# Kernel tuning notes

Hardware: AMD Instinct MI355X
Metric: run time of the kernel (lower is better)

Reference implementation:

```python
import jax, jax.numpy as jnp
import numpy as np

DIM = 1024
EXPANSION = 4
NUM_EXPERTS = 8
N_TOKENS = 4096
CAPACITY_FACTOR = 1.0  # also becomes the gate's k -> top-1 (bug-faithful)
EPS = 1e-6


def setup_inputs() -> dict:
    key = jax.random.key(0)
    ks = jax.random.split(key, 7)
    h = DIM * EXPANSION
    s = 0.02
    return {
        "x": jax.random.normal(ks[0], (N_TOKENS, DIM), dtype=jnp.float32),
        "w_gate": jax.random.normal(ks[1], (DIM, NUM_EXPERTS), dtype=jnp.float32) * s,
        "b_gate": jnp.zeros((NUM_EXPERTS,), dtype=jnp.float32),
        "w1": jax.random.normal(ks[2], (NUM_EXPERTS, DIM, h), dtype=jnp.float32) * s,
        "b1": jnp.zeros((NUM_EXPERTS, h), dtype=jnp.float32),
        "w2": jax.random.normal(ks[3], (NUM_EXPERTS, h, DIM), dtype=jnp.float32) * s,
        "b2": jnp.zeros((NUM_EXPERTS, DIM), dtype=jnp.float32),
    }


def fast_gelu(x):
    return x * jax.nn.sigmoid(1.702 * x)


def switch_gate(x, w_gate, b_gate):
    # x: [n, d] -> gate_scores: [n, e]
    gate_scores = jax.nn.softmax(x @ w_gate + b_gate, axis=-1)
    capacity = int(CAPACITY_FACTOR * x.shape[0])
    k = int(CAPACITY_FACTOR)  # SwitchMoE passes capacity_factor as k -> top-1
    _, top_k_idx = jax.lax.top_k(gate_scores, k)  # [n, k]
    mask = jnp.zeros_like(gate_scores).at[
        jnp.arange(x.shape[0])[:, None], top_k_idx
    ].set(1.0)
    masked = gate_scores * mask
    denom = masked.sum(axis=0, keepdims=True) + EPS  # [1, e]
    gate_scores = masked / denom * capacity
    # aux loss (use_aux_loss=True in SwitchMoE)
    load = gate_scores.sum(axis=0)               # [e]
    importance = gate_scores.sum(axis=1).mean()  # scalar
    loss = jnp.mean((load - importance) ** 2)
    return gate_scores, loss


def reference(x, w_gate, b_gate, w1, b1, w2, b2):
    gate_scores, loss = switch_gate(x, w_gate, b_gate)  # [n, e], scalar
    # dense compute-all-experts (faithful to the naive module)
    h = fast_gelu(jnp.einsum("nd,edh->enh", x, w1) + b1[:, None, :])  # [e, n, h]
    expert_out = jnp.einsum("enh,ehd->end", h, w2) + b2[:, None, :]   # [e, n, d]
    # weighted combine: sum_e gate[n,e] * expert_out[e,n,d]
    moe_output = jnp.einsum("ne,end->nd", gate_scores, expert_out)
    return moe_output, loss
```

## Files before the change

### kernel.cpp

```cpp
#include <hip/hip_runtime.h>
#include <hip/hip_bf16.h>
#include <math.h>

#define DIMK   1024
#define HDIM   4096
#define NEXP   8
#define NTOK   4096
#define EPSV   1e-6f

typedef __attribute__((ext_vector_type(4))) float  f32x4;
typedef __attribute__((ext_vector_type(8))) __bf16 bf16x8;
typedef __attribute__((ext_vector_type(4))) __bf16 bf16x4;

__device__ __forceinline__ __bf16 f2bf(float f) { return (__bf16)f; }

__device__ __forceinline__ void gload_lds16(const void* g, void* l) {
    __builtin_amdgcn_global_load_lds(
        (const __attribute__((address_space(1))) void*)g,
        (__attribute__((address_space(3))) void*)l, 16, 0, 0);
}

__global__ void init_kernel(int* counts, int* cursors, float* S) {
    int t = threadIdx.x;
    if (t < NEXP) { counts[t] = 0; cursors[t] = 0; S[t] = 0.0f; }
}

__global__ __launch_bounds__(256) void gate_kernel(
    const float* __restrict__ x, const float* __restrict__ wg,
    const float* __restrict__ bg,
    float* S, int* counts, float* score_top, int* texp)
{
    int n = blockIdx.x;
    int t = threadIdx.x;
    f32x4 xv = *(const f32x4*)(x + (size_t)n * DIMK + t * 4);

    float p[NEXP];
#pragma unroll
    for (int e = 0; e < NEXP; e++) p[e] = 0.0f;
#pragma unroll
    for (int j = 0; j < 4; j++) {
        int d = t * 4 + j;
        f32x4 wa = *(const f32x4*)(wg + (size_t)d * NEXP);
        f32x4 wb = *(const f32x4*)(wg + (size_t)d * NEXP + 4);
#pragma unroll
        for (int e = 0; e < 4; e++) { p[e] += xv[j] * wa[e]; p[e + 4] += xv[j] * wb[e]; }
    }
#pragma unroll
    for (int e = 0; e < NEXP; e++) {
#pragma unroll
        for (int off = 32; off > 0; off >>= 1)
            p[e] += __shfl_down(p[e], off, 64);
    }
    __shared__ float red[4][NEXP];
    int lane = t & 63, wv = t >> 6;
    if (lane == 0) {
#pragma unroll
        for (int e = 0; e < NEXP; e++) red[wv][e] = p[e];
    }
    __syncthreads();
    if (t == 0) {
        float l[NEXP]; float m = -1e30f;
#pragma unroll
        for (int e = 0; e < NEXP; e++) {
            l[e] = red[0][e] + red[1][e] + red[2][e] + red[3][e] + bg[e];
            m = fmaxf(m, l[e]);
        }
        float pe[NEXP]; float s = 0.0f;
#pragma unroll
        for (int e = 0; e < NEXP; e++) { pe[e] = __expf(l[e] - m); s += pe[e]; }
        int best = 0; float bv = pe[0];
#pragma unroll
        for (int e = 1; e < NEXP; e++) if (pe[e] > bv) { bv = pe[e]; best = e; }
        float sc = bv / s;
        score_top[n] = sc;
        texp[n] = best;
        atomicAdd(&S[best], sc);
        atomicAdd(&counts[best], 1);
    }
}

__global__ void finalize_kernel(const float* S, const int* counts,
                                int* offsets, float* loss_out)
{
    if (threadIdx.x == 0 && blockIdx.x == 0) {
        int off = 0;
        float loadv[NEXP]; float tot = 0.0f;
        for (int e = 0; e < NEXP; e++) { offsets[e] = off; off += counts[e]; }
        for (int e = 0; e < NEXP; e++) {
            loadv[e] = S[e] / (S[e] + EPSV) * (float)NTOK;
            tot += loadv[e];
        }
        float imp = tot / (float)NTOK;
        float loss = 0.0f;
        for (int e = 0; e < NEXP; e++) { float d = loadv[e] - imp; loss += d * d; }
        loss_out[0] = loss / (float)NEXP;
    }
}

__global__ __launch_bounds__(256) void assign_kernel(
    const int* __restrict__ texp, const float* __restrict__ score_top,
    const float* __restrict__ S, const int* __restrict__ offsets,
    int* cursors, int* perm, float* gatew)
{
    int n = blockIdx.x * 256 + threadIdx.x;
    int e = texp[n];
    int pos = atomicAdd(&cursors[e], 1);
    perm[offsets[e] + pos] = n;
    gatew[n] = score_top[n] / (S[e] + EPSV) * (float)NTOK;
}

__global__ __launch_bounds__(256) void bias_init_kernel(
    const int* __restrict__ texp, const float* __restrict__ gatew,
    const float* __restrict__ b2, float* __restrict__ out)
{
    int n = blockIdx.x;
    int t = threadIdx.x;
    int e = texp[n];
    float g = gatew[n];
    f32x4 b = *(const f32x4*)(b2 + (size_t)e * DIMK + t * 4);
    f32x4 o = { b.x * g, b.y * g, b.z * g, b.w * g };
    *(f32x4*)(out + (size_t)n * DIMK + t * 4) = o;
}

__global__ __launch_bounds__(256) void cvt_kernel(
    const float* __restrict__ x, __bf16* __restrict__ xb)
{
    size_t i = ((size_t)blockIdx.x * 256 + threadIdx.x) * 8;
    f32x4 a = *(const f32x4*)(x + i);
    f32x4 b = *(const f32x4*)(x + i + 4);
    bf16x8 w = { f2bf(a.x), f2bf(a.y), f2bf(a.z), f2bf(a.w),
                 f2bf(b.x), f2bf(b.y), f2bf(b.z), f2bf(b.w) };
    *(bf16x8*)(xb + i) = w;
}

__global__ __launch_bounds__(256) void transpose_kernel(
    const float* __restrict__ src, __bf16* __restrict__ dst, int K, int N)
{
    int tilesN = N >> 6;
    int per = (K >> 6) * tilesN;
    int e = blockIdx.x / per; int r = blockIdx.x % per;
    int tk = r / tilesN, tn = r % tilesN;
    const float* S = src + (size_t)e * K * N + (size_t)(tk << 6) * N + (tn << 6);
    __bf16* D = dst + (size_t)e * K * N + (size_t)(tn << 6) * K + (tk << 6);
    __shared__ __bf16 T[64 * 68];
    int t = threadIdx.x;
#pragma unroll
    for (int i = 0; i < 4; i++) {
        int ch = t + 256 * i;
        int k = ch >> 4, n4 = (ch & 15) << 2;
        f32x4 v = *(const f32x4*)(S + (size_t)k * N + n4);
#pragma unroll
        for (int j = 0; j < 4; j++) T[(n4 + j) * 68 + k] = f2bf(v[j]);
    }
    __syncthreads();
#pragma unroll
    for (int i = 0; i < 2; i++) {
        int o = t + 256 * i;
        int n = o >> 3, kc = o & 7;
        bf16x4 a = *(const bf16x4*)&T[n * 68 + kc * 8];
        bf16x4 b = *(const bf16x4*)&T[n * 68 + kc * 8 + 4];
        bf16x8 w = { a.x, a.y, a.z, a.w, b.x, b.y, b.z, b.w };
        *(bf16x8*)(D + (size_t)n * K + kc * 8) = w;
    }
}

__global__ __launch_bounds__(256) void gemm1_kernel(
    const __bf16* __restrict__ xbf, const __bf16* __restrict__ w1t,
    const float* __restrict__ b1,
    const int* __restrict__ perm, const int* __restrict__ counts,
    const int* __restrict__ offsets, __bf16* __restrict__ hbuf)
{
    int bx  = blockIdx.x;
    int e   = bx >> 10;
    int rem = bx & 1023;
    int mt  = rem >> 5, nt = rem & 31;
    int ce  = counts[e];
    int m0  = mt * 128;
    if (m0 >= ce) return;
    int off = offsets[e];
    int n0  = nt * 128;
    const __bf16* Bsrc = w1t + (size_t)e * DIMK * HDIM + (size_t)n0 * DIMK;

    __shared__ __bf16 As[128 * 64];
    __shared__ __bf16 Bs[128 * 64];

    int t = threadIdx.x;
    int lane = t & 63, wv = t >> 6;
    int wm = (wv >> 1) * 64, wn = (wv & 1) * 64;
    int lr = lane & 15, lq = lane >> 4;

    const __bf16* ag[4]; const __bf16* bg[4];
    __bf16 *al[4], *bl[4];
#pragma unroll
    for (int c = 0; c < 4; c++) {
        int s = c * 256 + t;
        int row = s >> 3, pc = s & 7;
        int gc = pc ^ (row & 7);
        int ri = m0 + row; if (ri >= ce) ri = ce - 1;
        ag[c] = xbf + (size_t)perm[off + ri] * DIMK + gc * 8;
        bg[c] = Bsrc + (size_t)row * DIMK + gc * 8;
        al[c] = As + s * 8;
        bl[c] = Bs + s * 8;
    }

    f32x4 acc[4][4];
#pragma unroll
    for (int mi = 0; mi < 4; mi++)
#pragma unroll
        for (int ni = 0; ni < 4; ni++) acc[mi][ni] = (f32x4)0.0f;

    for (int k0 = 0; k0 < DIMK; k0 += 64) {
#pragma unroll
        for (int c = 0; c < 4; c++) gload_lds16(ag[c], al[c]);
#pragma unroll
        for (int c = 0; c < 4; c++) gload_lds16(bg[c], bl[c]);
        __syncthreads();
#pragma unroll
        for (int ks = 0; ks < 2; ks++) {
            bf16x8 af[4], bfr[4];
#pragma unroll
            for (int i = 0; i < 4; i++) {
                int ra = wm + i * 16 + lr;
                af[i]  = *(const bf16x8*)(As + ra * 64 + (((ks * 4 + lq) ^ (ra & 7)) << 3));
                int rb = wn + i * 16 + lr;
                bfr[i] = *(const bf16x8*)(Bs + rb * 64 + (((ks * 4 + lq) ^ (rb & 7)) << 3));
            }
#pragma unroll
            for (int mi = 0; mi < 4; mi++)
#pragma unroll
                for (int ni = 0; ni < 4; ni++)
                    acc[mi][ni] = __builtin_amdgcn_mfma_f32_16x16x32_bf16(
                        af[mi], bfr[ni], acc[mi][ni], 0, 0, 0);
        }
        __syncthreads();
#pragma unroll
        for (int c = 0; c < 4; c++) { ag[c] += 64; bg[c] += 64; }
    }

    const float* b1e = b1 + (size_t)e * HDIM;
#pragma unroll
    for (int mi = 0; mi < 4; mi++) {
#pragma unroll
        for (int rr = 0; rr < 4; rr++) {
            int i = m0 + wm + mi * 16 + lq * 4 + rr;
            if (i < ce) {
                __bf16* hrow = hbuf + (size_t)(off + i) * HDIM;
#pragma unroll
                for (int ni = 0; ni < 4; ni++) {
                    int j = n0 + wn + ni * 16 + lr;
                    float v = acc[mi][ni][rr] + b1e[j];
                    v = v / (1.0f + __expf(-1.702f * v));
                    hrow[j] = f2bf(v);
                }
            }
        }
    }
}

__global__ __launch_bounds__(256) void gemm2_kernel(
    const __bf16* __restrict__ hbuf, const __bf16* __restrict__ w2t,
    const int* __restrict__ perm, const int* __restrict__ counts,
    const int* __restrict__ offsets, const float* __restrict__ gatew,
    float* __restrict__ out)
{
    int bx = blockIdx.x;
    int sk = bx & 1; int r = bx >> 1;
    int e = r >> 8; int rem = r & 255;
    int mt = rem >> 3, nt = rem & 7;
    int ce = counts[e];
    int m0 = mt * 128;
    if (m0 >= ce) return;
    int off = offsets[e];
    int n0 = nt * 128;
    int kbeg = sk * (HDIM / 2);
    const __bf16* Bsrc = w2t + (size_t)e * HDIM * DIMK + (size_t)n0 * HDIM;

    __shared__ __bf16 As[128 * 64];
    __shared__ __bf16 Bs[128 * 64];

    int t = threadIdx.x;
    int lane = t & 63, wv = t >> 6;
    int wm = (wv >> 1) * 64, wn = (wv & 1) * 64;
    int lr = lane & 15, lq = lane >> 4;

    const __bf16* ag[4]; const __bf16* bg[4];
    __bf16 *al[4], *bl[4];
#pragma unroll
    for (int c = 0; c < 4; c++) {
        int s = c * 256 + t;
        int row = s >> 3, pc = s & 7;
        int gc = pc ^ (row & 7);
        int ri = m0 + row; if (ri >= ce) ri = ce - 1;
        ag[c] = hbuf + (size_t)(off + ri) * HDIM + kbeg + gc * 8;
        bg[c] = Bsrc + (size_t)row * HDIM + kbeg + gc * 8;
        al[c] = As + s * 8;
        bl[c] = Bs + s * 8;
    }

    f32x4 acc[4][4];
#pragma unroll
    for (int mi = 0; mi < 4; mi++)
#pragma unroll
        for (int ni = 0; ni < 4; ni++) acc[mi][ni] = (f32x4)0.0f;

    for (int k0 = 0; k0 < HDIM / 2; k0 += 64) {
#pragma unroll
        for (int c = 0; c < 4; c++) gload_lds16(ag[c], al[c]);
#pragma unroll
        for (int c = 0; c < 4; c++) gload_lds16(bg[c], bl[c]);
        __syncthreads();
#pragma unroll
        for (int ks = 0; ks < 2; ks++) {
            bf16x8 af[4], bfr[4];
#pragma unroll
            for (int i = 0; i < 4; i++) {
                int ra = wm + i * 16 + lr;
                af[i]  = *(const bf16x8*)(As + ra * 64 + (((ks * 4 + lq) ^ (ra & 7)) << 3));
                int rb = wn + i * 16 + lr;
                bfr[i] = *(const bf16x8*)(Bs + rb * 64 + (((ks * 4 + lq) ^ (rb & 7)) << 3));
            }
#pragma unroll
            for (int mi = 0; mi < 4; mi++)
#pragma unroll
                for (int ni = 0; ni < 4; ni++)
                    acc[mi][ni] = __builtin_amdgcn_mfma_f32_16x16x32_bf16(
                        af[mi], bfr[ni], acc[mi][ni], 0, 0, 0);
        }
        __syncthreads();
#pragma unroll
        for (int c = 0; c < 4; c++) { ag[c] += 64; bg[c] += 64; }
    }

#pragma unroll
    for (int mi = 0; mi < 4; mi++) {
#pragma unroll
        for (int rr = 0; rr < 4; rr++) {
            int i = m0 + wm + mi * 16 + lq * 4 + rr;
            if (i < ce) {
                int tok = perm[off + i];
                float g = gatew[tok];
                float* orow = out + (size_t)tok * DIMK;
#pragma unroll
                for (int ni = 0; ni < 4; ni++) {
                    int j = n0 + wn + ni * 16 + lr;
                    atomicAdd(&orow[j], acc[mi][ni][rr] * g);
                }
            }
        }
    }
}

extern "C" void kernel_launch(void* const* d_in, const int* in_sizes, int n_in,
                              void* d_out, int out_size, void* d_ws, size_t ws_size,
                              hipStream_t stream)
{
    const float* x  = (const float*)d_in[0];
    const float* wg = (const float*)d_in[1];
    const float* bg = (const float*)d_in[2];
    const float* w1 = (const float*)d_in[3];
    const float* b1 = (const float*)d_in[4];
    const float* w2 = (const float*)d_in[5];
    const float* b2 = (const float*)d_in[6];
    float* out = (float*)d_out;

    char* wsb = (char*)d_ws;
    int*   counts  = (int*)  (wsb + 0);
    int*   cursors = (int*)  (wsb + 32);
    int*   offsets = (int*)  (wsb + 64);
    float* S       = (float*)(wsb + 96);
    float* score   = (float*)(wsb + 128);
    int*   texp    = (int*)  (wsb + 16512);
    int*   perm    = (int*)  (wsb + 32896);
    float* gatew   = (float*)(wsb + 49280);
    __bf16* hbuf   = (__bf16*)(wsb + 131072);
    __bf16* xbf    = (__bf16*)(wsb + 33685504);
    __bf16* w1t    = (__bf16*)(wsb + 42074112);
    __bf16* w2t    = (__bf16*)(wsb + 109182976);

    init_kernel<<<1, 64, 0, stream>>>(counts, cursors, S);
    gate_kernel<<<NTOK, 256, 0, stream>>>(x, wg, bg, S, counts, score, texp);
    finalize_kernel<<<1, 64, 0, stream>>>(S, counts, offsets, out + (size_t)NTOK * DIMK);
    assign_kernel<<<NTOK / 256, 256, 0, stream>>>(texp, score, S, offsets,
                                                  cursors, perm, gatew);
    bias_init_kernel<<<NTOK, 256, 0, stream>>>(texp, gatew, b2, out);
    cvt_kernel<<<(NTOK * DIMK) / (256 * 8), 256, 0, stream>>>(x, xbf);
    transpose_kernel<<<NEXP * 16 * 64, 256, 0, stream>>>(w1, w1t, DIMK, HDIM);
    transpose_kernel<<<NEXP * 64 * 16, 256, 0, stream>>>(w2, w2t, HDIM, DIMK);
    gemm1_kernel<<<NEXP * 32 * 32, 256, 0, stream>>>(xbf, w1t, b1, perm, counts,
                                                     offsets, hbuf);
    gemm2_kernel<<<NEXP * 32 * 8 * 2, 256, 0, stream>>>(hbuf, w2t, perm, counts,
                                                        offsets, gatew, out);
}
```

Baseline: 579.7 us.

## Double-buffer LDS tiles in both expert GEMM kernels to overlap loads with MFMA

Both expert GEMM kernels now keep two shared-memory buffers for the A and B tiles. Each loop iteration issues the async global-to-LDS load for the next K tile before running the MFMA work on the current tile, then swaps buffers after a single barrier. This is meant to hide global load latency behind matrix math instead of stalling at a barrier every step. It doubles LDS use per block to 64KB, which can lower how many blocks fit on each compute unit.

New measurement: 615.9 us. +6.2%, slower.

```diff
diff --git a/kernel.cpp b/kernel.cpp
--- a/kernel.cpp
+++ b/kernel.cpp
@@ -181,8 +181,8 @@
     int n0  = nt * 128;
     const __bf16* Bsrc = w1t + (size_t)e * DIMK * HDIM + (size_t)n0 * DIMK;
 
-    __shared__ __bf16 As[128 * 64];
-    __shared__ __bf16 Bs[128 * 64];
+    __shared__ __bf16 As[2][128 * 64];
+    __shared__ __bf16 Bs[2][128 * 64];
 
     int t = threadIdx.x;
     int lane = t & 63, wv = t >> 6;
@@ -190,7 +190,7 @@
     int lr = lane & 15, lq = lane >> 4;
 
     const __bf16* ag[4]; const __bf16* bg[4];
-    __bf16 *al[4], *bl[4];
+    int lofs[4];
 #pragma unroll
     for (int c = 0; c < 4; c++) {
         int s = c * 256 + t;
@@ -199,8 +199,7 @@
         int ri = m0 + row; if (ri >= ce) ri = ce - 1;
         ag[c] = xbf + (size_t)perm[off + ri] * DIMK + gc * 8;
         bg[c] = Bsrc + (size_t)row * DIMK + gc * 8;
-        al[c] = As + s * 8;
-        bl[c] = Bs + s * 8;
+        lofs[c] = s * 8;
     }
 
     f32x4 acc[4][4];
@@ -209,21 +208,36 @@
 #pragma unroll
         for (int ni = 0; ni < 4; ni++) acc[mi][ni] = (f32x4)0.0f;
 
-    for (int k0 = 0; k0 < DIMK; k0 += 64) {
-#pragma unroll
-        for (int c = 0; c < 4; c++) gload_lds16(ag[c], al[c]);
-#pragma unroll
-        for (int c = 0; c < 4; c++) gload_lds16(bg[c], bl[c]);
-        __syncthreads();
+#pragma unroll
+    for (int c = 0; c < 4; c++) {
+        gload_lds16(ag[c], &As[0][lofs[c]]);
+        gload_lds16(bg[c], &Bs[0][lofs[c]]);
+        ag[c] += 64; bg[c] += 64;
+    }
+    __syncthreads();
+
+    int cur = 0;
+    for (int t0 = 0; t0 < DIMK / 64; ++t0) {
+        if (t0 < DIMK / 64 - 1) {
+            int nxt = cur ^ 1;
+#pragma unroll
+            for (int c = 0; c < 4; c++) {
+                gload_lds16(ag[c], &As[nxt][lofs[c]]);
+                gload_lds16(bg[c], &Bs[nxt][lofs[c]]);
+                ag[c] += 64; bg[c] += 64;
+            }
+        }
+        const __bf16* Ab = &As[cur][0];
+        const __bf16* Bb = &Bs[cur][0];
 #pragma unroll
         for (int ks = 0; ks < 2; ks++) {
             bf16x8 af[4], bfr[4];
 #pragma unroll
             for (int i = 0; i < 4; i++) {
                 int ra = wm + i * 16 + lr;
-                af[i]  = *(const bf16x8*)(As + ra * 64 + (((ks * 4 + lq) ^ (ra & 7)) << 3));
+                af[i]  = *(const bf16x8*)(Ab + ra * 64 + (((ks * 4 + lq) ^ (ra & 7)) << 3));
                 int rb = wn + i * 16 + lr;
-                bfr[i] = *(const bf16x8*)(Bs + rb * 64 + (((ks * 4 + lq) ^ (rb & 7)) << 3));
+                bfr[i] = *(const bf16x8*)(Bb + rb * 64 + (((ks * 4 + lq) ^ (rb & 7)) << 3));
             }
 #pragma unroll
             for (int mi = 0; mi < 4; mi++)
@@ -233,8 +247,7 @@
                         af[mi], bfr[ni], acc[mi][ni], 0, 0, 0);
         }
         __syncthreads();
-#pragma unroll
-        for (int c = 0; c < 4; c++) { ag[c] += 64; bg[c] += 64; }
+        cur ^= 1;
     }
 
     const float* b1e = b1 + (size_t)e * HDIM;
@@ -275,8 +288,8 @@
     int kbeg = sk * (HDIM / 2);
     const __bf16* Bsrc = w2t + (size_t)e * HDIM * DIMK + (size_t)n0 * HDIM;
 
-    __shared__ __bf16 As[128 * 64];
-    __shared__ __bf16 Bs[128 * 64];
+    __shared__ __bf16 As[2][128 * 64];
+    __shared__ __bf16 Bs[2][128 * 64];
 
     int t = threadIdx.x;
     int lane = t & 63, wv = t >> 6;
@@ -284,7 +297,7 @@
     int lr = lane & 15, lq = lane >> 4;
 
     const __bf16* ag[4]; const __bf16* bg[4];
-    __bf16 *al[4], *bl[4];
+    int lofs[4];
 #pragma unroll
     for (int c = 0; c < 4; c++) {
         int s = c * 256 + t;
@@ -293,8 +306,7 @@
         int ri = m0 + row; if (ri >= ce) ri = ce - 1;
         ag[c] = hbuf + (size_t)(off + ri) * HDIM + kbeg + gc * 8;
         bg[c] = Bsrc + (size_t)row * HDIM + kbeg + gc * 8;
-        al[c] = As + s * 8;
-        bl[c] = Bs + s * 8;
+        lofs[c] = s * 8;
     }
 
     f32x4 acc[4][4];
@@ -303,21 +315,36 @@
 #pragma unroll
         for (int ni = 0; ni < 4; ni++) acc[mi][ni] = (f32x4)0.0f;
 
-    for (int k0 = 0; k0 < HDIM / 2; k0 += 64) {
-#pragma unroll
-        for (int c = 0; c < 4; c++) gload_lds16(ag[c], al[c]);
-#pragma unroll
-        for (int c = 0; c < 4; c++) gload_lds16(bg[c], bl[c]);
-        __syncthreads();
+#pragma unroll
+    for (int c = 0; c < 4; c++) {
+        gload_lds16(ag[c], &As[0][lofs[c]]);
+        gload_lds16(bg[c], &Bs[0][lofs[c]]);
+        ag[c] += 64; bg[c] += 64;
+    }
+    __syncthreads();
+
+    int cur = 0;
+    for (int t0 = 0; t0 < (HDIM / 2) / 64; ++t0) {
+        if (t0 < (HDIM / 2) / 64 - 1) {
+            int nxt = cur ^ 1;
+#pragma unroll
+            for (int c = 0; c < 4; c++) {
+                gload_lds16(ag[c], &As[nxt][lofs[c]]);
+                gload_lds16(bg[c], &Bs[nxt][lofs[c]]);
+                ag[c] += 64; bg[c] += 64;
+            }
+        }
+        const __bf16* Ab = &As[cur][0];
+        const __bf16* Bb = &Bs[cur][0];
 #pragma unroll
         for (int ks = 0; ks < 2; ks++) {
             bf16x8 af[4], bfr[4];
 #pragma unroll
             for (int i = 0; i < 4; i++) {
                 int ra = wm + i * 16 + lr;
-                af[i]  = *(const bf16x8*)(As + ra * 64 + (((ks * 4 + lq) ^ (ra & 7)) << 3));
+                af[i]  = *(const bf16x8*)(Ab + ra * 64 + (((ks * 4 + lq) ^ (ra & 7)) << 3));
                 int rb = wn + i * 16 + lr;
-                bfr[i] = *(const bf16x8*)(Bs + rb * 64 + (((ks * 4 + lq) ^ (rb & 7)) << 3));
+                bfr[i] = *(const bf16x8*)(Bb + rb * 64 + (((ks * 4 + lq) ^ (rb & 7)) << 3));
             }
 #pragma unroll
             for (int mi = 0; mi < 4; mi++)
@@ -327,8 +354,7 @@
                         af[mi], bfr[ni], acc[mi][ni], 0, 0, 0);
         }
         __syncthreads();
-#pragma unroll
-        for (int c = 0; c < 4; c++) { ag[c] += 64; bg[c] += 64; }
+        cur ^= 1;
     }
 
 #pragma unroll
```

## Rewrite expert GEMMs with 256x256 tiles and multi-stage LDS prefetch pipeline

Applied to the files above, without the earlier changes.

Both grouped expert GEMMs move from 128x128 tiles with 256 threads and a single LDS buffer to 256x256 tiles with 512 threads. The tile is split into four 128x128 quadrants that are double-buffered in LDS, so loads for upcoming k-steps are issued during MFMA work and gated with explicit vmcnt waits, barriers and setprio. The aim is to hide global-load latency and raise data reuse per block. The cost is coarser work granularity and much more LDS per block (128KB). GEMM2 also moves to a 4-way K split, which doubles the fp32 atomic adds into the output.

Result: slower. 596.3 us (+2.9%).

```diff
diff --git a/kernel.cpp b/kernel.cpp
--- a/kernel.cpp
+++ b/kernel.cpp
@@ -13,6 +13,7 @@
 typedef __attribute__((ext_vector_type(4))) __bf16 bf16x4;
 
 __device__ __forceinline__ __bf16 f2bf(float f) { return (__bf16)f; }
+__device__ __forceinline__ int imin(int a, int b) { return a < b ? a : b; }
 
 __device__ __forceinline__ void gload_lds16(const void* g, void* l) {
     __builtin_amdgcn_global_load_lds(
@@ -164,187 +165,241 @@
     }
 }
 
-__global__ __launch_bounds__(256) void gemm1_kernel(
+
+#define VM8 asm volatile("s_waitcnt vmcnt(8)" ::: "memory")
+#define VM6 asm volatile("s_waitcnt vmcnt(6)" ::: "memory")
+#define VM_NONE ((void)0)
+
+#define STG_A(BUF, H, KT) do { \
+    gload_lds16(agp[H][0] + (size_t)(KT) * 64, &As[BUF][H][(size_t)tid * 8]); \
+    gload_lds16(agp[H][1] + (size_t)(KT) * 64, &As[BUF][H][(size_t)(512 + tid) * 8]); } while (0)
+
+#define STG_B(BUF, H, KT) do { \
+    gload_lds16(bgp[H][0] + (size_t)(KT) * 64, &Bs[BUF][H][(size_t)tid * 8]); \
+    gload_lds16(bgp[H][1] + (size_t)(KT) * 64, &Bs[BUF][H][(size_t)(512 + tid) * 8]); } while (0)
+
+#define PHB(BUF, MH, NH, STG, VM) { \
+    bf16x8 Bf[2][2]; \
+    _Pragma("unroll") \
+    for (int ni_ = 0; ni_ < 2; ni_++) { \
+        int rb_ = wn32 + ni_ * 16 + lr; \
+        Bf[ni_][0] = *(const bf16x8*)(&Bs[BUF][NH][rb_ * 64 + (((lq) ^ (rb_ & 7)) << 3)]); \
+        Bf[ni_][1] = *(const bf16x8*)(&Bs[BUF][NH][rb_ * 64 + (((4 + lq) ^ (rb_ & 7)) << 3)]); \
+    } \
+    STG; \
+    __builtin_amdgcn_s_barrier(); \
+    asm volatile("s_waitcnt lgkmcnt(0)" ::: "memory"); \
+    __builtin_amdgcn_s_setprio(1); \
+    _Pragma("unroll") \
+    for (int ks_ = 0; ks_ < 2; ks_++) \
+    _Pragma("unroll") \
+    for (int mi_ = 0; mi_ < 4; mi_++) \
+    _Pragma("unroll") \
+    for (int ni_ = 0; ni_ < 2; ni_++) \
+        acc[MH][NH][mi_][ni_] = __builtin_amdgcn_mfma_f32_16x16x32_bf16( \
+            Af[mi_][ks_], Bf[ni_][ks_], acc[MH][NH][mi_][ni_], 0, 0, 0); \
+    __builtin_amdgcn_s_setprio(0); \
+    VM; \
+    __builtin_amdgcn_s_barrier(); \
+}
+
+#define PAIR(BUF, MH, STG1, VM1, STG2, VM2) { \
+    bf16x8 Af[4][2]; \
+    _Pragma("unroll") \
+    for (int mi_ = 0; mi_ < 4; mi_++) { \
+        int ra_ = wm64 + mi_ * 16 + lr; \
+        Af[mi_][0] = *(const bf16x8*)(&As[BUF][MH][ra_ * 64 + (((lq) ^ (ra_ & 7)) << 3)]); \
+        Af[mi_][1] = *(const bf16x8*)(&As[BUF][MH][ra_ * 64 + (((4 + lq) ^ (ra_ & 7)) << 3)]); \
+    } \
+    PHB(BUF, MH, 0, STG1, VM1); \
+    PHB(BUF, MH, 1, STG2, VM2); \
+}
+
+__global__ __launch_bounds__(512, 2) void gemm1_kernel(
     const __bf16* __restrict__ xbf, const __bf16* __restrict__ w1t,
     const float* __restrict__ b1,
     const int* __restrict__ perm, const int* __restrict__ counts,
     const int* __restrict__ offsets, __bf16* __restrict__ hbuf)
 {
     int bx  = blockIdx.x;
-    int e   = bx >> 10;
-    int rem = bx & 1023;
-    int mt  = rem >> 5, nt = rem & 31;
+    int e   = bx >> 8;
+    int rem = bx & 255;
+    int mt  = rem >> 4, nt = rem & 15;
     int ce  = counts[e];
-    int m0  = mt * 128;
+    int m0  = mt * 256;
     if (m0 >= ce) return;
     int off = offsets[e];
-    int n0  = nt * 128;
-    const __bf16* Bsrc = w1t + (size_t)e * DIMK * HDIM + (size_t)n0 * DIMK;
-
-    __shared__ __bf16 As[128 * 64];
-    __shared__ __bf16 Bs[128 * 64];
-
-    int t = threadIdx.x;
-    int lane = t & 63, wv = t >> 6;
-    int wm = (wv >> 1) * 64, wn = (wv & 1) * 64;
+    int n0  = nt * 256;
+    const __bf16* Bsrc = w1t + (size_t)e * DIMK * HDIM;
+
+    __shared__ __bf16 As[2][2][128 * 64];
+    __shared__ __bf16 Bs[2][2][128 * 64];
+
+    int tid  = threadIdx.x;
+    int lane = tid & 63, wid = tid >> 6;
+    int wm64 = (wid >> 2) * 64;
+    int wn32 = (wid & 3) * 32;
     int lr = lane & 15, lq = lane >> 4;
 
-    const __bf16* ag[4]; const __bf16* bg[4];
-    __bf16 *al[4], *bl[4];
-#pragma unroll
-    for (int c = 0; c < 4; c++) {
-        int s = c * 256 + t;
-        int row = s >> 3, pc = s & 7;
-        int gc = pc ^ (row & 7);
-        int ri = m0 + row; if (ri >= ce) ri = ce - 1;
-        ag[c] = xbf + (size_t)perm[off + ri] * DIMK + gc * 8;
-        bg[c] = Bsrc + (size_t)row * DIMK + gc * 8;
-        al[c] = As + s * 8;
-        bl[c] = Bs + s * 8;
-    }
-
-    f32x4 acc[4][4];
+    const __bf16* agp[2][2];
+    const __bf16* bgp[2][2];
+    {
+        int s0 = tid, s1 = 512 + tid;
+        int r0 = s0 >> 3, g0 = (s0 & 7) ^ (r0 & 7);
+        int r1 = s1 >> 3, g1 = (s1 & 7) ^ (r1 & 7);
+#pragma unroll
+        for (int h = 0; h < 2; h++) {
+            int ri0 = imin(m0 + h * 128 + r0, ce - 1);
+            int ri1 = imin(m0 + h * 128 + r1, ce - 1);
+            agp[h][0] = xbf + (size_t)perm[off + ri0] * DIMK + g0 * 8;
+            agp[h][1] = xbf + (size_t)perm[off + ri1] * DIMK + g1 * 8;
+            bgp[h][0] = Bsrc + (size_t)(n0 + h * 128 + r0) * DIMK + g0 * 8;
+            bgp[h][1] = Bsrc + (size_t)(n0 + h * 128 + r1) * DIMK + g1 * 8;
+        }
+    }
+
+    f32x4 acc[2][2][4][2];
+#pragma unroll
+    for (int a = 0; a < 2; a++)
+#pragma unroll
+    for (int b = 0; b < 2; b++)
+#pragma unroll
+    for (int c = 0; c < 4; c++)
+#pragma unroll
+    for (int d = 0; d < 2; d++) acc[a][b][c][d] = (f32x4)0.0f;
+
+    STG_A(0, 0, 0);
+    STG_B(0, 0, 0);
+    STG_A(0, 1, 0);
+    STG_B(0, 1, 0);
+    STG_A(1, 0, 1);
+    STG_B(1, 0, 1);
+    VM8;
+    __builtin_amdgcn_s_barrier();
+
+    const int NT = DIMK / 64;
+    for (int kt = 0; kt < NT; kt += 2) {
+        int k2 = imin(kt + 2, NT - 1);
+        int k3 = imin(kt + 3, NT - 1);
+        PAIR(0, 0, STG_A(1, 1, kt + 1), VM6, STG_B(1, 1, kt + 1), VM_NONE);
+        PAIR(0, 1, STG_A(0, 0, k2),  VM_NONE, STG_B(0, 0, k2),    VM8);
+        PAIR(1, 0, STG_A(0, 1, k2),     VM6,  STG_B(0, 1, k2),    VM_NONE);
+        PAIR(1, 1, STG_A(1, 0, k3),  VM_NONE, STG_B(1, 0, k3),    VM8);
+    }
+
+    const float* b1e = b1 + (size_t)e * HDIM;
+#pragma unroll
+    for (int Mh = 0; Mh < 2; Mh++)
 #pragma unroll
     for (int mi = 0; mi < 4; mi++)
 #pragma unroll
-        for (int ni = 0; ni < 4; ni++) acc[mi][ni] = (f32x4)0.0f;
-
-    for (int k0 = 0; k0 < DIMK; k0 += 64) {
-#pragma unroll
-        for (int c = 0; c < 4; c++) gload_lds16(ag[c], al[c]);
-#pragma unroll
-        for (int c = 0; c < 4; c++) gload_lds16(bg[c], bl[c]);
-        __syncthreads();
-#pragma unroll
-        for (int ks = 0; ks < 2; ks++) {
-            bf16x8 af[4], bfr[4];
-#pragma unroll
-            for (int i = 0; i < 4; i++) {
-                int ra = wm + i * 16 + lr;
-                af[i]  = *(const bf16x8*)(As + ra * 64 + (((ks * 4 + lq) ^ (ra & 7)) << 3));
-                int rb = wn + i * 16 + lr;
-                bfr[i] = *(const bf16x8*)(Bs + rb * 64 + (((ks * 4 + lq) ^ (rb & 7)) << 3));
+    for (int rr = 0; rr < 4; rr++) {
+        int i = m0 + Mh * 128 + wm64 + mi * 16 + lq * 4 + rr;
+        if (i < ce) {
+            __bf16* hrow = hbuf + (size_t)(off + i) * HDIM;
+#pragma unroll
+            for (int Nh = 0; Nh < 2; Nh++)
+#pragma unroll
+            for (int ni = 0; ni < 2; ni++) {
+                int j = n0 + Nh * 128 + wn32 + ni * 16 + lr;
+                float v = acc[Mh][Nh][mi][ni][rr] + b1e[j];
+                v = v / (1.0f + __expf(-1.702f * v));
+                hrow[j] = f2bf(v);
             }
-#pragma unroll
-            for (int mi = 0; mi < 4; mi++)
-#pragma unroll
-                for (int ni = 0; ni < 4; ni++)
-                    acc[mi][ni] = __builtin_amdgcn_mfma_f32_16x16x32_bf16(
-                        af[mi], bfr[ni], acc[mi][ni], 0, 0, 0);
-        }
-        __syncthreads();
-#pragma unroll
-        for (int c = 0; c < 4; c++) { ag[c] += 64; bg[c] += 64; }
-    }
-
-    const float* b1e = b1 + (size_t)e * HDIM;
-#pragma unroll
-    for (int mi = 0; mi < 4; mi++) {
-#pragma unroll
-        for (int rr = 0; rr < 4; rr++) {
-            int i = m0 + wm + mi * 16 + lq * 4 + rr;
-            if (i < ce) {
-                __bf16* hrow = hbuf + (size_t)(off + i) * HDIM;
-#pragma unroll
-                for (int ni = 0; ni < 4; ni++) {
-                    int j = n0 + wn + ni * 16 + lr;
-                    float v = acc[mi][ni][rr] + b1e[j];
-                    v = v / (1.0f + __expf(-1.702f * v));
-                    hrow[j] = f2bf(v);
-                }
-            }
-        }
-    }
-}
-
-__global__ __launch_bounds__(256) void gemm2_kernel(
+        }
+    }
+}
+
+__global__ __launch_bounds__(512, 2) void gemm2_kernel(
     const __bf16* __restrict__ hbuf, const __bf16* __restrict__ w2t,
     const int* __restrict__ perm, const int* __restrict__ counts,
     const int* __restrict__ offsets, const float* __restrict__ gatew,
     float* __restrict__ out)
 {
     int bx = blockIdx.x;
-    int sk = bx & 1; int r = bx >> 1;
-    int e = r >> 8; int rem = r & 255;
-    int mt = rem >> 3, nt = rem & 7;
+    int sk = bx & 3; int r = bx >> 2;
+    int e = r >> 6; int rem = r & 63;
+    int mt = rem >> 2, nt = rem & 3;
     int ce = counts[e];
-    int m0 = mt * 128;
+    int m0 = mt * 256;
     if (m0 >= ce) return;
     int off = offsets[e];
-    int n0 = nt * 128;
-    int kbeg = sk * (HDIM / 2);
-    const __bf16* Bsrc = w2t + (size_t)e * HDIM * DIMK + (size_t)n0 * HDIM;
-
-    __shared__ __bf16 As[128 * 64];
-    __shared__ __bf16 Bs[128 * 64];
-
-    int t = threadIdx.x;
-    int lane = t & 63, wv = t >> 6;
-    int wm = (wv >> 1) * 64, wn = (wv & 1) * 64;
+    int n0 = nt * 256;
+    int kbeg = sk * (HDIM / 4);
+    const __bf16* Bsrc = w2t + (size_t)e * HDIM * DIMK + kbeg;
+
+    __shared__ __bf16 As[2][2][128 * 64];
+    __shared__ __bf16 Bs[2][2][128 * 64];
+
+    int tid  = threadIdx.x;
+    int lane = tid & 63, wid = tid >> 6;
+    int wm64 = (wid >> 2) * 64;
+    int wn32 = (wid & 3) * 32;
     int lr = lane & 15, lq = lane >> 4;
 
-    const __bf16* ag[4]; const __bf16* bg[4];
-    __bf16 *al[4], *bl[4];
-#pragma unroll
-    for (int c = 0; c < 4; c++) {
-        int s = c * 256 + t;
-        int row = s >> 3, pc = s & 7;
-        int gc = pc ^ (row & 7);
-        int ri = m0 + row; if (ri >= ce) ri = ce - 1;
-        ag[c] = hbuf + (size_t)(off + ri) * HDIM + kbeg + gc * 8;
-        bg[c] = Bsrc + (size_t)row * HDIM + kbeg + gc * 8;
-        al[c] = As + s * 8;
-        bl[c] = Bs + s * 8;
-    }
-
-    f32x4 acc[4][4];
+    const __bf16* agp[2][2];
+    const __bf16* bgp[2][2];
+    {
+        int s0 = tid, s1 = 512 + tid;
+        int r0 = s0 >> 3, g0 = (s0 & 7) ^ (r0 & 7);
+        int r1 = s1 >> 3, g1 = (s1 & 7) ^ (r1 & 7);
+#pragma unroll
+        for (int h = 0; h < 2; h++) {
+            int ri0 = imin(m0 + h * 128 + r0, ce - 1);
+            int ri1 = imin(m0 + h * 128 + r1, ce - 1);
+            agp[h][0] = hbuf + (size_t)(off + ri0) * HDIM + kbeg + g0 * 8;
+            agp[h][1] = hbuf + (size_t)(off + ri1) * HDIM + kbeg + g1 * 8;
+            bgp[h][0] = Bsrc + (size_t)(n0 + h * 128 + r0) * HDIM + g0 * 8;
+            bgp[h][1] = Bsrc + (size_t)(n0 + h * 128 + r1) * HDIM + g1 * 8;
+        }
+    }
+
+    f32x4 acc[2][2][4][2];
+#pragma unroll
+    for (int a = 0; a < 2; a++)
+#pragma unroll
+    for (int b = 0; b < 2; b++)
+#pragma unroll
+    for (int c = 0; c < 4; c++)
+#pragma unroll
+    for (int d = 0; d < 2; d++) acc[a][b][c][d] = (f32x4)0.0f;
+
+    STG_A(0, 0, 0);
+    STG_B(0, 0, 0);
+    STG_A(0, 1, 0);
+    STG_B(0, 1, 0);
+    STG_A(1, 0, 1);
+    STG_B(1, 0, 1);
+    VM8;
+    __builtin_amdgcn_s_barrier();
+
+    const int NT = (HDIM / 4) / 64;
+    for (int kt = 0; kt < NT; kt += 2) {
+        int k2 = imin(kt + 2, NT - 1);
+        int k3 = imin(kt + 3, NT - 1);
+        PAIR(0, 0, STG_A(1, 1, kt + 1), VM6, STG_B(1, 1, kt + 1), VM_NONE);
+        PAIR(0, 1, STG_A(0, 0, k2),  VM_NONE, STG_B(0, 0, k2),    VM8);
+        PAIR(1, 0, STG_A(0, 1, k2),     VM6,  STG_B(0, 1, k2),    VM_NONE);
+        PAIR(1, 1, STG_A(1, 0, k3),  VM_NONE, STG_B(1, 0, k3),    VM8);
+    }
+
+#pragma unroll
+    for (int Mh = 0; Mh < 2; Mh++)
 #pragma unroll
     for (int mi = 0; mi < 4; mi++)
 #pragma unroll
-        for (int ni = 0; ni < 4; ni++) acc[mi][ni] = (f32x4)0.0f;
-
-    for (int k0 = 0; k0 < HDIM / 2; k0 += 64) {
-#pragma unroll
-        for (int c = 0; c < 4; c++) gload_lds16(ag[c], al[c]);
-#pragma unroll
-        for (int c = 0; c < 4; c++) gload_lds16(bg[c], bl[c]);
-        __syncthreads();
-#pragma unroll
-        for (int ks = 0; ks < 2; ks++) {
-            bf16x8 af[4], bfr[4];
-#pragma unroll
-            for (int i = 0; i < 4; i++) {
-                int ra = wm + i * 16 + lr;
-                af[i]  = *(const bf16x8*)(As + ra * 64 + (((ks * 4 + lq) ^ (ra & 7)) << 3));
-                int rb = wn + i * 16 + lr;
-                bfr[i] = *(const bf16x8*)(Bs + rb * 64 + (((ks * 4 + lq) ^ (rb & 7)) << 3));
-            }
-#pragma unroll
-            for (int mi = 0; mi < 4; mi++)
-#pragma unroll
-                for (int ni = 0; ni < 4; ni++)
-                    acc[mi][ni] = __builtin_amdgcn_mfma_f32_16x16x32_bf16(
-                        af[mi], bfr[ni], acc[mi][ni], 0, 0, 0);
-        }
-        __syncthreads();
-#pragma unroll
-        for (int c = 0; c < 4; c++) { ag[c] += 64; bg[c] += 64; }
-    }
-
-#pragma unroll
-    for (int mi = 0; mi < 4; mi++) {
-#pragma unroll
-        for (int rr = 0; rr < 4; rr++) {
-            int i = m0 + wm + mi * 16 + lq * 4 + rr;
-            if (i < ce) {
-                int tok = perm[off + i];
-                float g = gatew[tok];
-                float* orow = out + (size_t)tok * DIMK;
-#pragma unroll
-                for (int ni = 0; ni < 4; ni++) {
-                    int j = n0 + wn + ni * 16 + lr;
-                    atomicAdd(&orow[j], acc[mi][ni][rr] * g);
-                }
+    for (int rr = 0; rr < 4; rr++) {
+        int i = m0 + Mh * 128 + wm64 + mi * 16 + lq * 4 + rr;
+        if (i < ce) {
+            int tok = perm[off + i];
+            float g = gatew[tok];
+            float* orow = out + (size_t)tok * DIMK;
+#pragma unroll
+            for (int Nh = 0; Nh < 2; Nh++)
+#pragma unroll
+            for (int ni = 0; ni < 2; ni++) {
+                int j = n0 + Nh * 128 + wn32 + ni * 16 + lr;
+                atomicAdd(&orow[j], acc[Mh][Nh][mi][ni][rr] * g);
             }
         }
     }
@@ -386,8 +441,8 @@
     cvt_kernel<<<(NTOK * DIMK) / (256 * 8), 256, 0, stream>>>(x, xbf);
     transpose_kernel<<<NEXP * 16 * 64, 256, 0, stream>>>(w1, w1t, DIMK, HDIM);
     transpose_kernel<<<NEXP * 64 * 16, 256, 0, stream>>>(w2, w2t, HDIM, DIMK);
-    gemm1_kernel<<<NEXP * 32 * 32, 256, 0, stream>>>(xbf, w1t, b1, perm, counts,
+    gemm1_kernel<<<NEXP * 16 * 16, 512, 0, stream>>>(xbf, w1t, b1, perm, counts,
                                                      offsets, hbuf);
-    gemm2_kernel<<<NEXP * 32 * 8 * 2, 256, 0, stream>>>(hbuf, w2t, perm, counts,
+    gemm2_kernel<<<NEXP * 16 * 4 * 4, 512, 0, stream>>>(hbuf, w2t, perm, counts,
                                                         offsets, gatew, out);
 }
```

## Fuse prep kernels and make expert GEMMs loop over M tiles persistently

Applied to the files above, without the earlier changes.

The gate, x-to-bf16 conversion and both weight transposes now run in one prep kernel, with block ranges split by role. Assign and bias-init are merged into one per-token kernel. The two expert GEMMs launch fixed grids (2048 and 1024 blocks) whose blocks stride over M tiles, instead of one block per possible tile with most exiting early. This removes several launches and the cost of empty blocks, but a skewed expert load can leave the per-expert strided loops imbalanced.

New measurement: 576.1 us. No clear change (-0.6%).

```diff
diff --git a/kernel.cpp b/kernel.cpp
--- a/kernel.cpp
+++ b/kernel.cpp
@@ -25,14 +25,62 @@
     if (t < NEXP) { counts[t] = 0; cursors[t] = 0; S[t] = 0.0f; }
 }
 
-__global__ __launch_bounds__(256) void gate_kernel(
+__device__ __forceinline__ void transpose_body(
+    const float* __restrict__ src, __bf16* __restrict__ dst,
+    int K, int N, int r, __bf16* T)
+{
+    int tilesN = N >> 6;
+    int per = (K >> 6) * tilesN;
+    int e = r / per; int rr = r % per;
+    int tk = rr / tilesN, tn = rr % tilesN;
+    const float* S = src + (size_t)e * K * N + (size_t)(tk << 6) * N + (tn << 6);
+    __bf16* D = dst + (size_t)e * K * N + (size_t)(tn << 6) * K + (tk << 6);
+    int t = threadIdx.x;
+#pragma unroll
+    for (int i = 0; i < 4; i++) {
+        int ch = t + 256 * i;
+        int k = ch >> 4, n4 = (ch & 15) << 2;
+        f32x4 v = *(const f32x4*)(S + (size_t)k * N + n4);
+#pragma unroll
+        for (int j = 0; j < 4; j++) T[(n4 + j) * 68 + k] = f2bf(v[j]);
+    }
+    __syncthreads();
+#pragma unroll
+    for (int i = 0; i < 2; i++) {
+        int o = t + 256 * i;
+        int n = o >> 3, kc = o & 7;
+        bf16x4 a = *(const bf16x4*)&T[n * 68 + kc * 8];
+        bf16x4 b = *(const bf16x4*)&T[n * 68 + kc * 8 + 4];
+        bf16x8 w = { a.x, a.y, a.z, a.w, b.x, b.y, b.z, b.w };
+        *(bf16x8*)(D + (size_t)n * K + kc * 8) = w;
+    }
+}
+
+__global__ __launch_bounds__(256) void prep_kernel(
     const float* __restrict__ x, const float* __restrict__ wg,
     const float* __restrict__ bg,
-    float* S, int* counts, float* score_top, int* texp)
-{
-    int n = blockIdx.x;
+    float* S, int* counts, float* score_top, int* texp,
+    __bf16* __restrict__ xb,
+    const float* __restrict__ w1, __bf16* __restrict__ w1t,
+    const float* __restrict__ w2, __bf16* __restrict__ w2t)
+{
+    __shared__ __bf16 T[64 * 68];
+    __shared__ float red[4][NEXP];
+    int bx = blockIdx.x;
+
+    if (bx >= NTOK) {
+        int r = bx - NTOK;
+        if (r < 8192) transpose_body(w1, w1t, DIMK, HDIM, r, T);
+        else          transpose_body(w2, w2t, HDIM, DIMK, r - 8192, T);
+        return;
+    }
+
+    int n = bx;
     int t = threadIdx.x;
     f32x4 xv = *(const f32x4*)(x + (size_t)n * DIMK + t * 4);
+
+    bf16x4 xw = { f2bf(xv.x), f2bf(xv.y), f2bf(xv.z), f2bf(xv.w) };
+    *(bf16x4*)(xb + (size_t)n * DIMK + t * 4) = xw;
 
     float p[NEXP];
 #pragma unroll
@@ -51,7 +99,6 @@
         for (int off = 32; off > 0; off >>= 1)
             p[e] += __shfl_down(p[e], off, 64);
     }
-    __shared__ float red[4][NEXP];
     int lane = t & 63, wv = t >> 6;
     if (lane == 0) {
 #pragma unroll
@@ -97,71 +144,24 @@
     }
 }
 
-__global__ __launch_bounds__(256) void assign_kernel(
+__global__ __launch_bounds__(256) void assign_bias_kernel(
     const int* __restrict__ texp, const float* __restrict__ score_top,
     const float* __restrict__ S, const int* __restrict__ offsets,
-    int* cursors, int* perm, float* gatew)
-{
-    int n = blockIdx.x * 256 + threadIdx.x;
+    int* cursors, int* perm, float* gatew,
+    const float* __restrict__ b2, float* __restrict__ out)
+{
+    int n = blockIdx.x;
+    int t = threadIdx.x;
     int e = texp[n];
-    int pos = atomicAdd(&cursors[e], 1);
-    perm[offsets[e] + pos] = n;
-    gatew[n] = score_top[n] / (S[e] + EPSV) * (float)NTOK;
-}
-
-__global__ __launch_bounds__(256) void bias_init_kernel(
-    const int* __restrict__ texp, const float* __restrict__ gatew,
-    const float* __restrict__ b2, float* __restrict__ out)
-{
-    int n = blockIdx.x;
-    int t = threadIdx.x;
-    int e = texp[n];
-    float g = gatew[n];
+    float g = score_top[n] / (S[e] + EPSV) * (float)NTOK;
+    if (t == 0) {
+        int pos = atomicAdd(&cursors[e], 1);
+        perm[offsets[e] + pos] = n;
+        gatew[n] = g;
+    }
     f32x4 b = *(const f32x4*)(b2 + (size_t)e * DIMK + t * 4);
     f32x4 o = { b.x * g, b.y * g, b.z * g, b.w * g };
     *(f32x4*)(out + (size_t)n * DIMK + t * 4) = o;
-}
-
-__global__ __launch_bounds__(256) void cvt_kernel(
-    const float* __restrict__ x, __bf16* __restrict__ xb)
-{
-    size_t i = ((size_t)blockIdx.x * 256 + threadIdx.x) * 8;
-    f32x4 a = *(const f32x4*)(x + i);
-    f32x4 b = *(const f32x4*)(x + i + 4);
-    bf16x8 w = { f2bf(a.x), f2bf(a.y), f2bf(a.z), f2bf(a.w),
-                 f2bf(b.x), f2bf(b.y), f2bf(b.z), f2bf(b.w) };
-    *(bf16x8*)(xb + i) = w;
-}
-
-__global__ __launch_bounds__(256) void transpose_kernel(
-    const float* __restrict__ src, __bf16* __restrict__ dst, int K, int N)
-{
-    int tilesN = N >> 6;
-    int per = (K >> 6) * tilesN;
-    int e = blockIdx.x / per; int r = blockIdx.x % per;
-    int tk = r / tilesN, tn = r % tilesN;
-    const float* S = src + (size_t)e * K * N + (size_t)(tk << 6) * N + (tn << 6);
-    __bf16* D = dst + (size_t)e * K * N + (size_t)(tn << 6) * K + (tk << 6);
-    __shared__ __bf16 T[64 * 68];
-    int t = threadIdx.x;
-#pragma unroll
-    for (int i = 0; i < 4; i++) {
-        int ch = t + 256 * i;
-        int k = ch >> 4, n4 = (ch & 15) << 2;
-        f32x4 v = *(const f32x4*)(S + (size_t)k * N + n4);
-#pragma unroll
-        for (int j = 0; j < 4; j++) T[(n4 + j) * 68 + k] = f2bf(v[j]);
-    }
-    __syncthreads();
-#pragma unroll
-    for (int i = 0; i < 2; i++) {
-        int o = t + 256 * i;
-        int n = o >> 3, kc = o & 7;
-        bf16x4 a = *(const bf16x4*)&T[n * 68 + kc * 8];
-        bf16x4 b = *(const bf16x4*)&T[n * 68 + kc * 8 + 4];
-        bf16x8 w = { a.x, a.y, a.z, a.w, b.x, b.y, b.z, b.w };
-        *(bf16x8*)(D + (size_t)n * K + kc * 8) = w;
-    }
 }
 
 __global__ __launch_bounds__(256) void gemm1_kernel(
@@ -171,12 +171,9 @@
     const int* __restrict__ offsets, __bf16* __restrict__ hbuf)
 {
     int bx  = blockIdx.x;
-    int e   = bx >> 10;
-    int rem = bx & 1023;
-    int mt  = rem >> 5, nt = rem & 31;
+    int sub = bx & 255;
+    int e   = sub >> 5, nt = sub & 31;
     int ce  = counts[e];
-    int m0  = mt * 128;
-    if (m0 >= ce) return;
     int off = offsets[e];
     int n0  = nt * 128;
     const __bf16* Bsrc = w1t + (size_t)e * DIMK * HDIM + (size_t)n0 * DIMK;
@@ -189,68 +186,77 @@
     int wm = (wv >> 1) * 64, wn = (wv & 1) * 64;
     int lr = lane & 15, lq = lane >> 4;
 
-    const __bf16* ag[4]; const __bf16* bg[4];
     __bf16 *al[4], *bl[4];
 #pragma unroll
     for (int c = 0; c < 4; c++) {
         int s = c * 256 + t;
-        int row = s >> 3, pc = s & 7;
-        int gc = pc ^ (row & 7);
-        int ri = m0 + row; if (ri >= ce) ri = ce - 1;
-        ag[c] = xbf + (size_t)perm[off + ri] * DIMK + gc * 8;
-        bg[c] = Bsrc + (size_t)row * DIMK + gc * 8;
         al[c] = As + s * 8;
         bl[c] = Bs + s * 8;
     }
 
-    f32x4 acc[4][4];
-#pragma unroll
-    for (int mi = 0; mi < 4; mi++)
-#pragma unroll
-        for (int ni = 0; ni < 4; ni++) acc[mi][ni] = (f32x4)0.0f;
-
-    for (int k0 = 0; k0 < DIMK; k0 += 64) {
-#pragma unroll
-        for (int c = 0; c < 4; c++) gload_lds16(ag[c], al[c]);
-#pragma unroll
-        for (int c = 0; c < 4; c++) gload_lds16(bg[c], bl[c]);
-        __syncthreads();
-#pragma unroll
-        for (int ks = 0; ks < 2; ks++) {
-            bf16x8 af[4], bfr[4];
-#pragma unroll
-            for (int i = 0; i < 4; i++) {
-                int ra = wm + i * 16 + lr;
-                af[i]  = *(const bf16x8*)(As + ra * 64 + (((ks * 4 + lq) ^ (ra & 7)) << 3));
-                int rb = wn + i * 16 + lr;
-                bfr[i] = *(const bf16x8*)(Bs + rb * 64 + (((ks * 4 + lq) ^ (rb & 7)) << 3));
+    for (int mt = bx >> 8; mt * 128 < ce; mt += 8) {
+        int m0 = mt * 128;
+
+        const __bf16* ag[4]; const __bf16* bg[4];
+#pragma unroll
+        for (int c = 0; c < 4; c++) {
+            int s = c * 256 + t;
+            int row = s >> 3, pc = s & 7;
+            int gc = pc ^ (row & 7);
+            int ri = m0 + row; if (ri >= ce) ri = ce - 1;
+            ag[c] = xbf + (size_t)perm[off + ri] * DIMK + gc * 8;
+            bg[c] = Bsrc + (size_t)row * DIMK + gc * 8;
+        }
+
+        f32x4 acc[4][4];
+#pragma unroll
+        for (int mi = 0; mi < 4; mi++)
+#pragma unroll
+            for (int ni = 0; ni < 4; ni++) acc[mi][ni] = (f32x4)0.0f;
+
+        for (int k0 = 0; k0 < DIMK; k0 += 64) {
+#pragma unroll
+            for (int c = 0; c < 4; c++) gload_lds16(ag[c], al[c]);
+#pragma unroll
+            for (int c = 0; c < 4; c++) gload_lds16(bg[c], bl[c]);
+            __syncthreads();
+#pragma unroll
+            for (int ks = 0; ks < 2; ks++) {
+                bf16x8 af[4], bfr[4];
+#pragma unroll
+                for (int i = 0; i < 4; i++) {
+                    int ra = wm + i * 16 + lr;
+                    af[i]  = *(const bf16x8*)(As + ra * 64 + (((ks * 4 + lq) ^ (ra & 7)) << 3));
+                    int rb = wn + i * 16 + lr;
+                    bfr[i] = *(const bf16x8*)(Bs + rb * 64 + (((ks * 4 + lq) ^ (rb & 7)) << 3));
+                }
+#pragma unroll
+                for (int mi = 0; mi < 4; mi++)
+#pragma unroll
+                    for (int ni = 0; ni < 4; ni++)
+                        acc[mi][ni] = __builtin_amdgcn_mfma_f32_16x16x32_bf16(
+                            af[mi], bfr[ni], acc[mi][ni], 0, 0, 0);
             }
-#pragma unroll
-            for (int mi = 0; mi < 4; mi++)
-#pragma unroll
-                for (int ni = 0; ni < 4; ni++)
-                    acc[mi][ni] = __builtin_amdgcn_mfma_f32_16x16x32_bf16(
-                        af[mi], bfr[ni], acc[mi][ni], 0, 0, 0);
-        }
-        __syncthreads();
-#pragma unroll
-        for (int c = 0; c < 4; c++) { ag[c] += 64; bg[c] += 64; }
-    }
-
-    const float* b1e = b1 + (size_t)e * HDIM;
-#pragma unroll
-    for (int mi = 0; mi < 4; mi++) {
-#pragma unroll
-        for (int rr = 0; rr < 4; rr++) {
-            int i = m0 + wm + mi * 16 + lq * 4 + rr;
-            if (i < ce) {
-                __bf16* hrow = hbuf + (size_t)(off + i) * HDIM;
-#pragma unroll
-                for (int ni = 0; ni < 4; ni++) {
-                    int j = n0 + wn + ni * 16 + lr;
-                    float v = acc[mi][ni][rr] + b1e[j];
-                    v = v / (1.0f + __expf(-1.702f * v));
-                    hrow[j] = f2bf(v);
+            __syncthreads();
+#pragma unroll
+            for (int c = 0; c < 4; c++) { ag[c] += 64; bg[c] += 64; }
+        }
+
+        const float* b1e = b1 + (size_t)e * HDIM;
+#pragma unroll
+        for (int mi = 0; mi < 4; mi++) {
+#pragma unroll
+            for (int rr = 0; rr < 4; rr++) {
+                int i = m0 + wm + mi * 16 + lq * 4 + rr;
+                if (i < ce) {
+                    __bf16* hrow = hbuf + (size_t)(off + i) * HDIM;
+#pragma unroll
+                    for (int ni = 0; ni < 4; ni++) {
+                        int j = n0 + wn + ni * 16 + lr;
+                        float v = acc[mi][ni][rr] + b1e[j];
+                        v = v / (1.0f + __expf(-1.702f * v));
+                        hrow[j] = f2bf(v);
+                    }
                 }
             }
         }
@@ -263,15 +269,14 @@
     const int* __restrict__ offsets, const float* __restrict__ gatew,
     float* __restrict__ out)
 {
-    int bx = blockIdx.x;
-    int sk = bx & 1; int r = bx >> 1;
-    int e = r >> 8; int rem = r & 255;
-    int mt = rem >> 3, nt = rem & 7;
-    int ce = counts[e];
-    int m0 = mt * 128;
-    if (m0 >= ce) return;
+    int bx  = blockIdx.x;
+    int sub = bx & 127;
+    int e   = sub >> 4;
+    int nt  = (sub >> 1) & 7;
+    int sk  = sub & 1;
+    int ce  = counts[e];
     int off = offsets[e];
-    int n0 = nt * 128;
+    int n0  = nt * 128;
     int kbeg = sk * (HDIM / 2);
     const __bf16* Bsrc = w2t + (size_t)e * HDIM * DIMK + (size_t)n0 * HDIM;
 
@@ -283,67 +288,76 @@
     int wm = (wv >> 1) * 64, wn = (wv & 1) * 64;
     int lr = lane & 15, lq = lane >> 4;
 
-    const __bf16* ag[4]; const __bf16* bg[4];
     __bf16 *al[4], *bl[4];
 #pragma unroll
     for (int c = 0; c < 4; c++) {
         int s = c * 256 + t;
-        int row = s >> 3, pc = s & 7;
-        int gc = pc ^ (row & 7);
-        int ri = m0 + row; if (ri >= ce) ri = ce - 1;
-        ag[c] = hbuf + (size_t)(off + ri) * HDIM + kbeg + gc * 8;
-        bg[c] = Bsrc + (size_t)row * HDIM + kbeg + gc * 8;
         al[c] = As + s * 8;
         bl[c] = Bs + s * 8;
     }
 
-    f32x4 acc[4][4];
-#pragma unroll
-    for (int mi = 0; mi < 4; mi++)
-#pragma unroll
-        for (int ni = 0; ni < 4; ni++) acc[mi][ni] = (f32x4)0.0f;
-
-    for (int k0 = 0; k0 < HDIM / 2; k0 += 64) {
-#pragma unroll
-        for (int c = 0; c < 4; c++) gload_lds16(ag[c], al[c]);
-#pragma unroll
-        for (int c = 0; c < 4; c++) gload_lds16(bg[c], bl[c]);
-        __syncthreads();
-#pragma unroll
-        for (int ks = 0; ks < 2; ks++) {
-            bf16x8 af[4], bfr[4];
-#pragma unroll
-            for (int i = 0; i < 4; i++) {
-                int ra = wm + i * 16 + lr;
-                af[i]  = *(const bf16x8*)(As + ra * 64 + (((ks * 4 + lq) ^ (ra & 7)) << 3));
-                int rb = wn + i * 16 + lr;
-                bfr[i] = *(const bf16x8*)(Bs + rb * 64 + (((ks * 4 + lq) ^ (rb & 7)) << 3));
+    for (int mt = bx >> 7; mt * 128 < ce; mt += 8) {
+        int m0 = mt * 128;
+
+        const __bf16* ag[4]; const __bf16* bg[4];
+#pragma unroll
+        for (int c = 0; c < 4; c++) {
+            int s = c * 256 + t;
+            int row = s >> 3, pc = s & 7;
+            int gc = pc ^ (row & 7);
+            int ri = m0 + row; if (ri >= ce) ri = ce - 1;
+            ag[c] = hbuf + (size_t)(off + ri) * HDIM + kbeg + gc * 8;
+            bg[c] = Bsrc + (size_t)row * HDIM + kbeg + gc * 8;
+        }
+
+        f32x4 acc[4][4];
+#pragma unroll
+        for (int mi = 0; mi < 4; mi++)
+#pragma unroll
+            for (int ni = 0; ni < 4; ni++) acc[mi][ni] = (f32x4)0.0f;
+
+        for (int k0 = 0; k0 < HDIM / 2; k0 += 64) {
+#pragma unroll
+            for (int c = 0; c < 4; c++) gload_lds16(ag[c], al[c]);
+#pragma unroll
+            for (int c = 0; c < 4; c++) gload_lds16(bg[c], bl[c]);
+            __syncthreads();
+#pragma unroll
+            for (int ks = 0; ks < 2; ks++) {
+                bf16x8 af[4], bfr[4];
+#pragma unroll
+                for (int i = 0; i < 4; i++) {
+                    int ra = wm + i * 16 + lr;
+                    af[i]  = *(const bf16x8*)(As + ra * 64 + (((ks * 4 + lq) ^ (ra & 7)) << 3));
+                    int rb = wn + i * 16 + lr;
+                    bfr[i] = *(const bf16x8*)(Bs + rb * 64 + (((ks * 4 + lq) ^ (rb & 7)) << 3));
+                }
+#pragma unroll
+                for (int mi = 0; mi < 4; mi++)
+#pragma unroll
+                    for (int ni = 0; ni < 4; ni++)
+                        acc[mi][ni] = __builtin_amdgcn_mfma_f32_16x16x32_bf16(
+                            af[mi], bfr[ni], acc[mi][ni], 0, 0, 0);
             }
-#pragma unroll
-            for (int mi = 0; mi < 4; mi++)
-#pragma unroll
-                for (int ni = 0; ni < 4; ni++)
-                    acc[mi][ni] = __builtin_amdgcn_mfma_f32_16x16x32_bf16(
-                        af[mi], bfr[ni], acc[mi][ni], 0, 0, 0);
-        }
-        __syncthreads();
-#pragma unroll
-        for (int c = 0; c < 4; c++) { ag[c] += 64; bg[c] += 64; }
-    }
-
-#pragma unroll
-    for (int mi = 0; mi < 4; mi++) {
-#pragma unroll
-        for (int rr = 0; rr < 4; rr++) {
-            int i = m0 + wm + mi * 16 + lq * 4 + rr;
-            if (i < ce) {
-                int tok = perm[off + i];
-                float g = gatew[tok];
-                float* orow = out + (size_t)tok * DIMK;
-#pragma unroll
-                for (int ni = 0; ni < 4; ni++) {
-                    int j = n0 + wn + ni * 16 + lr;
-                    atomicAdd(&orow[j], acc[mi][ni][rr] * g);
+            __syncthreads();
+#pragma unroll
+            for (int c = 0; c < 4; c++) { ag[c] += 64; bg[c] += 64; }
+        }
+
+#pragma unroll
+        for (int mi = 0; mi < 4; mi++) {
+#pragma unroll
+            for (int rr = 0; rr < 4; rr++) {
+                int i = m0 + wm + mi * 16 + lq * 4 + rr;
+                if (i < ce) {
+                    int tok = perm[off + i];
+                    float g = gatew[tok];
+                    float* orow = out + (size_t)tok * DIMK;
+#pragma unroll
+                    for (int ni = 0; ni < 4; ni++) {
+                        int j = n0 + wn + ni * 16 + lr;
+                        atomicAdd(&orow[j], acc[mi][ni][rr] * g);
+                    }
                 }
             }
         }
@@ -378,16 +392,13 @@
     __bf16* w2t    = (__bf16*)(wsb + 109182976);
 
     init_kernel<<<1, 64, 0, stream>>>(counts, cursors, S);
-    gate_kernel<<<NTOK, 256, 0, stream>>>(x, wg, bg, S, counts, score, texp);
+    prep_kernel<<<NTOK + 8192 + 8192, 256, 0, stream>>>(
+        x, wg, bg, S, counts, score, texp, xbf, w1, w1t, w2, w2t);
     finalize_kernel<<<1, 64, 0, stream>>>(S, counts, offsets, out + (size_t)NTOK * DIMK);
-    assign_kernel<<<NTOK / 256, 256, 0, stream>>>(texp, score, S, offsets,
-                                                  cursors, perm, gatew);
-    bias_init_kernel<<<NTOK, 256, 0, stream>>>(texp, gatew, b2, out);
-    cvt_kernel<<<(NTOK * DIMK) / (256 * 8), 256, 0, stream>>>(x, xbf);
-    transpose_kernel<<<NEXP * 16 * 64, 256, 0, stream>>>(w1, w1t, DIMK, HDIM);
-    transpose_kernel<<<NEXP * 64 * 16, 256, 0, stream>>>(w2, w2t, HDIM, DIMK);
-    gemm1_kernel<<<NEXP * 32 * 32, 256, 0, stream>>>(xbf, w1t, b1, perm, counts,
-                                                     offsets, hbuf);
-    gemm2_kernel<<<NEXP * 32 * 8 * 2, 256, 0, stream>>>(hbuf, w2t, perm, counts,
-                                                        offsets, gatew, out);
-}
+    assign_bias_kernel<<<NTOK, 256, 0, stream>>>(texp, score, S, offsets,
+                                                 cursors, perm, gatew, b2, out);
+    gemm1_kernel<<<2048, 256, 0, stream>>>(xbf, w1t, b1, perm, counts,
+                                           offsets, hbuf);
+    gemm2_kernel<<<1024, 256, 0, stream>>>(hbuf, w2t, perm, counts,
+                                           offsets, gatew, out);
+}
```
